# Kernel tuning notes

Measured on AMD Instinct MI355X. Metric: run time of the kernel, lower is better.

## Reference

```python
import jax, jax.numpy as jnp
import numpy as np

B_, C_, H_, W_ = 8, 128, 64, 64
OUT_ = 128
D_MODEL = C_ // 4        # 32, per-chunk channels fed to Mamba
D_STATE = 16
D_CONV = 4
D_INNER = 2 * D_MODEL    # expand=2 -> 64
DT_RANK = max(1, -(-D_MODEL // 16))  # ceil(32/16)=2
SE_RED = 2


def _ln(x, g, b):
    m = x.mean(-1, keepdims=True)
    v = jnp.var(x, axis=-1, keepdims=True)
    return (x - m) / jnp.sqrt(v + 1e-5) * g + b


def _mamba(u, in_W, conv_W, conv_b, xproj_W, dt_W, dt_b, A_log, D_p, out_W):
    # u: (B, L, d_model)
    Bsz, L, _ = u.shape
    xz = u @ in_W.T                                   # (B,L,2*d_inner)
    x, z = jnp.split(xz, 2, axis=-1)
    # causal depthwise conv1d along L
    xc = jnp.swapaxes(x, 1, 2)                        # (B,d_inner,L)
    xc = jax.lax.conv_general_dilated(
        xc, conv_W, (1,), [(D_CONV - 1, 0)],
        feature_group_count=D_INNER,
        dimension_numbers=('NCH', 'OIH', 'NCH'))
    x = jax.nn.silu(jnp.swapaxes(xc + conv_b[None, :, None], 1, 2))
    x_dbl = x @ xproj_W.T                             # (B,L,dt_rank+2*d_state)
    dt, Bm, Cm = jnp.split(x_dbl, [DT_RANK, DT_RANK + D_STATE], axis=-1)
    dt = jax.nn.softplus(dt @ dt_W.T + dt_b)          # (B,L,d_inner)
    A = -jnp.exp(A_log)                               # (d_inner,d_state)
    dA = jnp.exp(dt[..., None] * A)                   # (B,L,d_inner,d_state)
    dBu = dt[..., None] * Bm[:, :, None, :] * x[..., None]

    def step(h, inp):
        dA_t, dBu_t, C_t = inp
        h = dA_t * h + dBu_t                          # (B,d_inner,d_state)
        return h, jnp.einsum('bds,bs->bd', h, C_t)

    h0 = jnp.zeros((Bsz, D_INNER, D_STATE), dtype=x.dtype)
    _, ys = jax.lax.scan(step, h0, (jnp.swapaxes(dA, 0, 1), jnp.swapaxes(dBu, 0, 1), jnp.swapaxes(Cm, 0, 1)))
    y = jnp.swapaxes(ys, 0, 1) + x * D_p
    y = y * jax.nn.silu(z)
    return y @ out_W.T


def _branch(xi, skip_scale, se_W1, se_W2, mp):
    M1 = _mamba(xi, *mp)                              # (B,L,c)
    M2 = skip_scale * xi
    # SE: adaptive avg-pool over spatial == mean over tokens; cat over channels
    y = jnp.concatenate([M1, M2], axis=-1).mean(axis=1)   # (B,2c)
    y = jax.nn.sigmoid(jax.nn.relu(y @ se_W1.T) @ se_W2.T)
    g1, g2 = jnp.split(y, 2, axis=-1)
    return g1[:, None, :] * M1 + g2[:, None, :] * M2


def _pvm(x, norm_g, norm_b, proj_W, proj_b, skip_scale, se_W1, se_W2,
         in_W, conv_W, conv_b, xproj_W, dt_W, dt_b, A_log, D_p, out_W):
    B, C, H, W = x.shape
    L = H * W
    xf = jnp.swapaxes(x.reshape(B, C, L), 1, 2)       # (B,L,C)
    xn = _ln(xf, norm_g, norm_b)
    mp = (in_W, conv_W, conv_b, xproj_W, dt_W, dt_b, A_log, D_p, out_W)
    outs = [_branch(c, skip_scale, se_W1, se_W2, mp) for c in jnp.split(xn, 4, axis=2)]
    xm = jnp.concatenate(outs, axis=2)                # (B,L,C)
    xm = _ln(xm, norm_g, norm_b)
    xm = xm @ proj_W.T + proj_b                       # (B,L,out)
    return jnp.swapaxes(xm, 1, 2).reshape(B, proj_W.shape[0], H, W)


def setup_inputs():
    key = jax.random.key(0)
    ks = jax.random.split(key, 10)
    p = {}
    p['x'] = jax.random.normal(ks[0], (B_, C_, H_, W_), jnp.float32)
    p['norm_g'] = jnp.ones((C_,), jnp.float32)
    p['norm_b'] = jnp.zeros((C_,), jnp.float32)
    p['proj_W'] = jax.random.normal(ks[1], (OUT_, C_), jnp.float32) * 0.05
    p['proj_b'] = jnp.zeros((OUT_,), jnp.float32)
    p['skip_scale'] = jnp.ones((1,), jnp.float32)
    p['se_W1'] = jax.random.normal(ks[2], (SE_RED, 2 * D_MODEL), jnp.float32) * 0.1
    p['se_W2'] = jax.random.normal(ks[3], (2 * D_MODEL, SE_RED), jnp.float32) * 0.1
    p['in_W'] = jax.random.normal(ks[4], (2 * D_INNER, D_MODEL), jnp.float32) * 0.1
    p['conv_W'] = jax.random.normal(ks[5], (D_INNER, 1, D_CONV), jnp.float32) * 0.2
    p['conv_b'] = jnp.zeros((D_INNER,), jnp.float32)
    p['xproj_W'] = jax.random.normal(ks[6], (DT_RANK + 2 * D_STATE, D_INNER), jnp.float32) * 0.1
    p['dt_W'] = jax.random.normal(ks[7], (D_INNER, DT_RANK), jnp.float32) * 0.1
    p['dt_b'] = jnp.full((D_INNER,), -4.6, jnp.float32)  # softplus(-4.6) ~ 0.01 init dt
    p['A_log'] = jnp.log(jnp.broadcast_to(jnp.arange(1.0, D_STATE + 1.0, dtype=jnp.float32), (D_INNER, D_STATE)))
    p['D_p'] = jnp.ones((D_INNER,), jnp.float32)
    p['out_W'] = jax.random.normal(ks[8], (D_MODEL, D_INNER), jnp.float32) * 0.1
    return p


def reference(x, norm_g, norm_b, proj_W, proj_b, skip_scale, se_W1, se_W2,
              in_W, conv_W, conv_b, xproj_W, dt_W, dt_b, A_log, D_p, out_W):
    return _pvm(x, norm_g, norm_b, proj_W, proj_b, skip_scale, se_W1, se_W2,
                in_W, conv_W, conv_b, xproj_W, dt_W, dt_b, A_log, D_p, out_W)
```

## Files before the change

kernel.cpp:

```cpp
#include <hip/hip_runtime.h>
#include <math.h>

typedef _Float16 h16;

#define DEV static __device__ __forceinline__

constexpr int B_ = 8, C_ = 128, L_ = 4096, OUT_ = 128;
constexpr int NCH = 4, DM = 32, DS = 16, DI = 64;
constexpr int NI = 32;
constexpr int NSEG = 128;
constexpr int SL = L_ / NSEG;

DEV float sigmoidf_(float x) { return 1.f / (1.f + __expf(-x)); }
DEV float siluf_(float x) { return x * sigmoidf_(x); }
DEV float softplusf_(float x) { return (x > 20.f) ? x : __logf(1.f + __expf(x)); }

template <int CTRL>
DEV float dpp_add_(float x) {
  int v = __builtin_amdgcn_update_dpp(0, __float_as_int(x), CTRL, 0xf, 0xf, false);
  return x + __int_as_float(v);
}

typedef __attribute__((ext_vector_type(8))) _Float16 f16x8;
typedef __attribute__((ext_vector_type(4))) _Float16 f16x4;
typedef __attribute__((ext_vector_type(4))) float f32x4;

DEV void powladder_(float E, float* out) {
  float E2 = E * E;
  float E4 = E2 * E2;
  float E8 = E4 * E4;
  float E3 = E2 * E;
  out[0] = E;       out[1] = E2;      out[2] = E3;      out[3] = E4;
  out[4] = E4 * E;  out[5] = E4 * E2; out[6] = E4 * E3; out[7] = E8;
  out[8] = E8 * E;  out[9] = E8 * E2; out[10] = E8 * E3; out[11] = E8 * E4;
  out[12] = E8 * out[4]; out[13] = E8 * out[5]; out[14] = E8 * out[6];
  out[15] = E8 * E8;
}

DEV void powladder8_(float E, float* out) {
  float E2 = E * E, E3 = E2 * E, E4 = E2 * E2;
  out[0] = E; out[1] = E2; out[2] = E3; out[3] = E4;
  out[4] = E4 * E; out[5] = E4 * E2; out[6] = E4 * E3; out[7] = E4 * E4;
}

__global__ __launch_bounds__(256) void k0_wcvt(const float* __restrict__ in_W,
                                               const float* __restrict__ xproj_W,
                                               h16* __restrict__ WH) {
  int tid = blockIdx.x * 256 + threadIdx.x;
  if (tid < 4096) {
    WH[tid] = (h16)in_W[tid];
  } else if (tid < 4096 + 48 * 64) {
    int j = tid - 4096;
    int r = j >> 6;
    WH[tid] = (r < 34) ? (h16)xproj_W[r * 64 + (j & 63)] : (h16)0.f;
  }
}

__global__ __launch_bounds__(256) void k1_ln(const float* __restrict__ x,
                                             const float* __restrict__ gn,
                                             const float* __restrict__ bn,
                                             float* __restrict__ XN,
                                             h16* __restrict__ XNH,
                                             float* __restrict__ SUMXN) {
  int bid = blockIdx.x;
  int b = bid >> 6, tile = bid & 63;
  int t0 = tile * 64;
  int tid = threadIdx.x;
  __shared__ float xT[128][65];
  __shared__ float gnS[128], bnS[128];
  __shared__ float red[256];
  if (tid < 128) { gnS[tid] = gn[tid]; bnS[tid] = bn[tid]; }
  for (int k = tid; k < 8192; k += 256) {
    int c = k >> 6, tt = k & 63;
    xT[c][tt] = x[((size_t)(b * C_ + c)) * L_ + t0 + tt];
  }
  __syncthreads();
  {
    int tok = tid >> 2, q = tid & 3;
    float s = 0.f, qq = 0.f;
#pragma unroll
    for (int j = 0; j < 32; ++j) {
      float v = xT[q + 4 * j][tok];
      s += v; qq += v * v;
    }
    s = dpp_add_<0xB1>(s); qq = dpp_add_<0xB1>(qq);
    s = dpp_add_<0x4E>(s); qq = dpp_add_<0x4E>(qq);
    float m = s * (1.f / 128.f);
    float var = qq * (1.f / 128.f) - m * m;
    float rs = rsqrtf(var + 1e-5f);
#pragma unroll
    for (int j = 0; j < 32; ++j) {
      int c = q + 4 * j;
      float v = xT[c][tok];
      xT[c][tok] = (v - m) * rs * gnS[c] + bnS[c];
    }
  }
  __syncthreads();
  float acc = 0.f;
  int cfix = tid & 127;
  for (int k = tid; k < 8192; k += 256) {
    int tt = k >> 7, c = k & 127;
    float v = xT[c][tt];
    XN[((size_t)(b * L_ + t0 + tt)) * C_ + c] = v;
    acc += v;
  }
  for (int k = tid; k < 1024; k += 256) {
    int tt = k >> 4, c8 = (k & 15) * 8;
    f16x8 hv;
#pragma unroll
    for (int j = 0; j < 8; ++j) hv[j] = (_Float16)xT[c8 + j][tt];
    *(f16x8*)&XNH[((size_t)(b * L_ + t0 + tt)) * C_ + c8] = hv;
  }
  red[tid] = acc;
  __syncthreads();
  if (tid < 128) atomicAdd(&SUMXN[b * C_ + cfix], red[tid] + red[tid + 128]);
}

__global__ __launch_bounds__(256) void k2_prep(
    const h16* __restrict__ WH, const float* __restrict__ conv_W,
    const float* __restrict__ conv_b, const float* __restrict__ dt_W,
    const float* __restrict__ dt_b, const float* __restrict__ A_log,
    const h16* __restrict__ XNH, h16* __restrict__ SX2, h16* __restrict__ SDT2,
    h16* __restrict__ SB2, h16* __restrict__ SC2, h16* __restrict__ SZ2,
    float* __restrict__ Pp, float* __restrict__ Qp) {
  int bid = blockIdx.x;
  int i = bid >> 6, tile = bid & 63;
  int b = i >> 2, ch = i & 3;
  int t0 = tile * 64;
  int tid = threadIdx.x;
  int w = __builtin_amdgcn_readfirstlane(tid >> 6);
  int lane = tid & 63;

  __shared__ __attribute__((aligned(16))) union {
    struct {
      _Float16 uH[80][40];
      _Float16 w1H[64][40];
    } s;
    float xdS[64][36];
    _Float16 zL[64][88];
  } U;
  __shared__ __attribute__((aligned(16))) _Float16 preH[80][66];
  __shared__ __attribute__((aligned(16))) _Float16 xH[64][72];
  __shared__ __attribute__((aligned(16))) _Float16 w2H[48][72];
  __shared__ float convWS[64][4];
  __shared__ float dtWS[64][2];
  __shared__ float dtbS[64], cbS[64];

  convWS[tid >> 2][tid & 3] = conv_W[tid];
  if (tid < 128) dtWS[tid >> 1][tid & 1] = dt_W[tid];
  if (tid < 64) { dtbS[tid] = dt_b[tid]; cbS[tid] = conv_b[tid]; }
  const h16* xnh = XNH + (size_t)b * L_ * C_ + ch * DM;
  for (int k = tid; k < 320; k += 256) {
    int r = k >> 2, c8 = (k & 3) * 8;
    int tg = t0 - 3 + r;
    f16x8 v = {0, 0, 0, 0, 0, 0, 0, 0};
    if (r < 67 && tg >= 0) v = *(const f16x8*)&xnh[(size_t)tg * C_ + c8];
    *(f16x8*)&U.s.uH[r][c8] = v;
  }
  {
    int r = tid >> 2, c8 = (tid & 3) * 8;
    *(f16x8*)&U.s.w1H[r][c8] = *(const f16x8*)&WH[r * 32 + c8];
  }
  for (int k = tid; k < 384; k += 256) {
    int r = k >> 3, c8 = (k & 7) * 8;
    *(f16x8*)&w2H[r][c8] = *(const f16x8*)&WH[4096 + r * 64 + c8];
  }
  __syncthreads();

  int rsel = lane & 15, ksel = (lane >> 4) * 8;
  {
    int nt = w;
    f16x8 bf = *(const f16x8*)&U.s.w1H[nt * 16 + rsel][ksel];
    int row0q = (lane >> 4) << 2;
    int col = nt * 16 + rsel;
#pragma unroll
    for (int mt = 0; mt < 5; ++mt) {
      f16x8 af = *(const f16x8*)&U.s.uH[mt * 16 + rsel][ksel];
      f32x4 acc = {0.f, 0.f, 0.f, 0.f};
      acc = __builtin_amdgcn_mfma_f32_16x16x32_f16(af, bf, acc, 0, 0, 0);
      int row0 = mt * 16 + row0q;
#pragma unroll
      for (int r = 0; r < 4; ++r) preH[row0 + r][col] = (_Float16)acc[r];
    }
  }
  f32x4 zacc[4];
  {
    f16x8 bf = *(const f16x8*)&U.s.uH[3 + w * 16 + rsel][ksel];
#pragma unroll
    for (int mt = 0; mt < 4; ++mt) {
      f16x8 af = *(const f16x8*)&WH[(size_t)(64 + mt * 16 + rsel) * 32 + ksel];
      f32x4 acc = {0.f, 0.f, 0.f, 0.f};
      zacc[mt] = __builtin_amdgcn_mfma_f32_16x16x32_f16(af, bf, acc, 0, 0, 0);
    }
  }
  __syncthreads();

  h16* SXp = SX2 + ((size_t)i * L_ + t0) * DI;
  for (int k = tid; k < 4096; k += 256) {
    int r = k >> 6, d = k & 63;
    float v = cbS[d];
#pragma unroll
    for (int j = 0; j < 4; ++j) v = fmaf(convWS[d][j], (float)preH[r + j][d], v);
    v = siluf_(v);
    xH[r][d] = (_Float16)v;
    SXp[(size_t)r * DI + d] = (h16)v;
  }
  __syncthreads();

  {
    int mt = w;
    f16x8 a0 = *(const f16x8*)&xH[mt * 16 + rsel][ksel];
    f16x8 a1 = *(const f16x8*)&xH[mt * 16 + rsel][32 + ksel];
    int row0 = mt * 16 + ((lane >> 4) << 2);
#pragma unroll
    for (int nt = 0; nt < 3; ++nt) {
      f16x8 b0 = *(const f16x8*)&w2H[nt * 16 + rsel][ksel];
      f16x8 b1 = *(const f16x8*)&w2H[nt * 16 + rsel][32 + ksel];
      f32x4 acc = {0.f, 0.f, 0.f, 0.f};
      acc = __builtin_amdgcn_mfma_f32_16x16x32_f16(a0, b0, acc, 0, 0, 0);
      acc = __builtin_amdgcn_mfma_f32_16x16x32_f16(a1, b1, acc, 0, 0, 0);
      int col = nt * 16 + rsel;
      if (col < 34) {
#pragma unroll
        for (int r = 0; r < 4; ++r) U.xdS[row0 + r][col] = acc[r];
      }
    }
  }
  __syncthreads();

  h16* dtL = (h16*)&preH[0][0];
  h16* SDTp = SDT2 + ((size_t)i * L_ + t0) * DI;
  for (int k = tid; k < 4096; k += 256) {
    int d = k & 63, r = k >> 6;
    float raw = fmaf(U.xdS[r][0], dtWS[d][0], fmaf(U.xdS[r][1], dtWS[d][1], dtbS[d]));
    float dtv = softplusf_(raw);
    dtL[r * 66 + d] = (_Float16)dtv;
    SDTp[(size_t)r * DI + d] = (h16)dtv;
  }
  h16* SBp = SB2 + ((size_t)i * L_ + t0) * DS;
  h16* SCp = SC2 + ((size_t)i * L_ + t0) * DS;
  for (int k = tid; k < 1024; k += 256) {
    int s = k & 15, r = k >> 4;
    SBp[(size_t)r * DS + s] = (h16)U.xdS[r][2 + s];
    SCp[(size_t)r * DS + s] = (h16)U.xdS[r][18 + s];
  }
  __syncthreads();

  {
    int seg = w >> 1, shalf = w & 1;
    int s0 = shalf * 8;
    float Av[16];
#pragma unroll
    for (int s = 0; s < 16; ++s) Av[s] = -__expf(A_log[lane * 16 + s]);
    float A0 = Av[0];
    bool okf = true;
#pragma unroll
    for (int s = 0; s < 16; ++s)
      okf &= fabsf(Av[s] - (float)(s + 1) * A0) <= 1e-4f * fabsf(Av[s]);
    int fastp = __all(okf ? 1 : 0);
    float h[8];
#pragma unroll
    for (int j = 0; j < 8; ++j) h[j] = 0.f;
    float sdt = 0.f;
    int rowbase = seg * SL;
    for (int t = 0; t < SL; ++t) {
      int row = rowbase + t;
      float dt = (float)dtL[row * 66 + lane];
      float xv = (float)xH[row][lane];
      float dtx = dt * xv;
      float dA[8];
      if (fastp) {
        powladder8_(__expf(A0 * dt), dA);
        if (shalf) {
          float E8 = dA[7];
#pragma unroll
          for (int j = 0; j < 8; ++j) dA[j] *= E8;
        }
      } else {
#pragma unroll
        for (int j = 0; j < 8; ++j) dA[j] = __expf(Av[s0 + j] * dt);
      }
      const float* brow = &U.xdS[row][2 + s0];
#pragma unroll
      for (int j = 0; j < 8; ++j) h[j] = fmaf(dA[j], h[j], dtx * brow[j]);
      sdt += dt;
    }
    float P[8];
    if (fastp) {
      powladder8_(__expf(A0 * sdt), P);
      if (shalf) {
        float E8 = P[7];
#pragma unroll
        for (int j = 0; j < 8; ++j) P[j] *= E8;
      }
    } else {
#pragma unroll
      for (int j = 0; j < 8; ++j) P[j] = __expf(Av[s0 + j] * sdt);
    }
    int segg = tile * 2 + seg;
    size_t base = (((size_t)i * DI + lane) * NSEG + segg) * DS + s0;
    *(float4*)(Pp + base) = *(float4*)&P[0];
    *(float4*)(Pp + base + 4) = *(float4*)&P[4];
    *(float4*)(Qp + base) = *(float4*)&h[0];
    *(float4*)(Qp + base + 4) = *(float4*)&h[4];
  }
  __syncthreads();

  {
    int tok = w * 16 + rsel;
    int zq = (lane >> 4) << 2;
#pragma unroll
    for (int mt = 0; mt < 4; ++mt) {
      f16x4 pk;
#pragma unroll
      for (int r = 0; r < 4; ++r) pk[r] = (_Float16)siluf_(zacc[mt][r]);
      *(f16x4*)&U.zL[tok][mt * 16 + zq] = pk;
    }
  }
  __syncthreads();
  h16* SZp = SZ2 + ((size_t)i * L_ + t0) * DI;
  for (int k = tid; k < 512; k += 256) {
    int r = k >> 3, dblk = (k & 7) * 8;
    f16x8 v = *(const f16x8*)&U.zL[r][dblk];
    *(f16x8*)&SZp[(size_t)r * DI + dblk] = v;
  }
}

__global__ __launch_bounds__(256) void k3b_comb(float* __restrict__ Pp,
                                                const float* __restrict__ Qp) {
  int g = blockIdx.x * 256 + threadIdx.x;
  int s = g & 15;
  int r = g >> 4;
  size_t base = (size_t)r * NSEG * DS + s;
  float H = 0.f;
  for (int sb = 0; sb < NSEG; sb += 8) {
    float Pv[8], Qv[8];
#pragma unroll
    for (int j = 0; j < 8; ++j) {
      size_t a = base + (size_t)(sb + j) * DS;
      Pv[j] = Pp[a];
      Qv[j] = Qp[a];
    }
#pragma unroll
    for (int j = 0; j < 8; ++j) {
      size_t a = base + (size_t)(sb + j) * DS;
      Pp[a] = H;
      H = fmaf(Pv[j], H, Qv[j]);
    }
  }
}

__global__ __launch_bounds__(256) void k3c_scan(
    const float* __restrict__ A_log, const h16* __restrict__ SDT2,
    const h16* __restrict__ SX2, const h16* __restrict__ SB2,
    const h16* __restrict__ SC2, const h16* __restrict__ SZ2,
    const float* __restrict__ D_p, const float* __restrict__ H0p,
    h16* __restrict__ YS2, float* __restrict__ SUMYF) {
  int bid = blockIdx.x;
  int i = bid >> 5, sg = bid & 31;
  int tid = threadIdx.x;
  int w = tid >> 6, lane = tid & 63;
  int seg = sg * 4 + w;
  int t0 = seg * SL;
  __shared__ float rowS[4][SL][36];
  {
    int tk = lane & 31, hf = lane >> 5;
    const h16* p = (hf ? SC2 : SB2) + ((size_t)i * L_ + t0 + tk) * DS;
    float4 r0 = *(const float4*)p;
    float4 r1 = *(const float4*)(p + 8);
    const h16* hp0 = (const h16*)&r0;
    const h16* hp1 = (const h16*)&r1;
#pragma unroll
    for (int s = 0; s < 8; ++s) {
      rowS[w][tk][hf * 16 + s] = (float)hp0[s];
      rowS[w][tk][hf * 16 + 8 + s] = (float)hp1[s];
    }
  }
  __syncthreads();
  float Av[16];
#pragma unroll
  for (int s = 0; s < 16; ++s) Av[s] = -__expf(A_log[lane * 16 + s]);
  float A0 = Av[0];
  bool okf = true;
#pragma unroll
  for (int s = 0; s < 16; ++s) okf &= fabsf(Av[s] - (float)(s + 1) * A0) <= 1e-4f * fabsf(Av[s]);
  int fastp = __all(okf ? 1 : 0);
  float Dp = D_p[lane];
  float h[16];
  {
    size_t base = (((size_t)i * DI + lane) * NSEG + seg) * DS;
#pragma unroll
    for (int j = 0; j < 4; ++j) *(float4*)&h[4 * j] = *(const float4*)(H0p + base + 4 * j);
  }
  const h16* pdt = SDT2 + ((size_t)i * L_ + t0) * DI + lane;
  const h16* pxx = SX2 + ((size_t)i * L_ + t0) * DI + lane;
  const h16* pzz = SZ2 + ((size_t)i * L_ + t0) * DI + lane;
  h16* pys = YS2 + ((size_t)i * L_ + t0) * DI + lane;
  float dtc = (float)pdt[0], xvc = (float)pxx[0], zvc = (float)pzz[0];
  float sum = 0.f;
  for (int t = 0; t < SL; ++t) {
    float dt = dtc, xv = xvc, zv = zvc;
    if (t < SL - 1) {
      dtc = (float)pdt[(t + 1) * DI];
      xvc = (float)pxx[(t + 1) * DI];
      zvc = (float)pzz[(t + 1) * DI];
    }
    const float* row = &rowS[w][t][0];
    float Bv[16], Cv[16];
#pragma unroll
    for (int j = 0; j < 4; ++j) {
      *(float4*)&Bv[4 * j] = *(const float4*)(row + 4 * j);
      *(float4*)&Cv[4 * j] = *(const float4*)(row + 16 + 4 * j);
    }
    float dtx = dt * xv;
    float dA[16];
    if (fastp) {
      powladder_(__expf(A0 * dt), dA);
    } else {
#pragma unroll
      for (int s = 0; s < 16; ++s) dA[s] = __expf(Av[s] * dt);
    }
    float y0 = 0.f, y1 = 0.f, y2 = 0.f, y3 = 0.f;
#pragma unroll
    for (int s = 0; s < 16; s += 4) {
      h[s] = fmaf(dA[s], h[s], dtx * Bv[s]);       y0 = fmaf(h[s], Cv[s], y0);
      h[s + 1] = fmaf(dA[s + 1], h[s + 1], dtx * Bv[s + 1]); y1 = fmaf(h[s + 1], Cv[s + 1], y1);
      h[s + 2] = fmaf(dA[s + 2], h[s + 2], dtx * Bv[s + 2]); y2 = fmaf(h[s + 2], Cv[s + 2], y2);
      h[s + 3] = fmaf(dA[s + 3], h[s + 3], dtx * Bv[s + 3]); y3 = fmaf(h[s + 3], Cv[s + 3], y3);
    }
    float y = (y0 + y1) + (y2 + y3);
    float yf = fmaf(xv, Dp, y) * zv;
    pys[(size_t)t * DI] = (h16)yf;
    sum += yf;
  }
  atomicAdd(&SUMYF[i * DI + lane], sum);
}

__global__ __launch_bounds__(64) void k4_gates(
    const float* __restrict__ out_W, const float* __restrict__ se_W1,
    const float* __restrict__ se_W2, const float* __restrict__ skip_p,
    const float* __restrict__ SUMYF, const float* __restrict__ SUMXN,
    float* __restrict__ GATES) {
  int i = blockIdx.x;
  int b = i >> 2, ch = i & 3;
  int tid = threadIdx.x;
  __shared__ float syS[64], catS[64], seS[2];
  syS[tid] = SUMYF[i * DI + tid];
  __syncthreads();
  float invL = 1.f / (float)L_;
  if (tid < 32) {
    float acc = 0.f;
#pragma unroll
    for (int dd = 0; dd < 64; ++dd) acc = fmaf(syS[dd], out_W[tid * 64 + dd], acc);
    catS[tid] = acc * invL;
  } else {
    int c = tid - 32;
    catS[tid] = skip_p[0] * SUMXN[b * C_ + ch * DM + c] * invL;
  }
  __syncthreads();
  if (tid < 2) {
    float acc = 0.f;
#pragma unroll
    for (int k = 0; k < 64; ++k) acc = fmaf(catS[k], se_W1[tid * 64 + k], acc);
    seS[tid] = fmaxf(acc, 0.f);
  }
  __syncthreads();
  float gg = fmaf(seS[0], se_W2[tid * 2 + 0], seS[1] * se_W2[tid * 2 + 1]);
  GATES[i * DI + tid] = sigmoidf_(gg);
}

__global__ __launch_bounds__(256) void k56_comb_proj(
    const float* __restrict__ out_W, const float* __restrict__ skip_p,
    const float* __restrict__ GATES, const h16* __restrict__ YS2,
    const float* __restrict__ gn, const float* __restrict__ bn,
    const float* __restrict__ proj_W, const float* __restrict__ proj_b,
    const float* __restrict__ XN, float* __restrict__ out) {
  int bid = blockIdx.x;
  int b = bid >> 6, tile = bid & 63;
  int t0 = tile * 64;
  int tid = threadIdx.x;
  int w = __builtin_amdgcn_readfirstlane(tid >> 6);
  int lane = tid & 63;
  __shared__ __attribute__((aligned(16))) union {
    float xmS[64][132];
    _Float16 projH[128][136];
  } U;
  __shared__ __attribute__((aligned(16))) union {
    struct {
      _Float16 yH[64][72];
      _Float16 owH[32][72];
    } pre;
    _Float16 xmH[64][136];
  } V;
  __shared__ float gAll[4][64];
  __shared__ float gnS[128], bnS[128];

  if (tid < 128) { gnS[tid] = gn[tid]; bnS[tid] = bn[tid]; }
  const float* xm = XN + (size_t)b * L_ * C_;
  for (int k = tid; k < 8192; k += 256) {
    int tt = k >> 7, c = k & 127;
    U.xmS[tt][c] = xm[(size_t)(t0 + tt) * C_ + c];
  }
  if (tid < 256) gAll[tid >> 6][tid & 63] = GATES[(b * 4 + (tid >> 6)) * DI + (tid & 63)];
  for (int k = tid; k < 2048; k += 256) V.pre.owH[k >> 6][k & 63] = (_Float16)out_W[k];

  int rsel = lane & 15, ksel = (lane >> 4) * 8;
  float skip = skip_p[0];
  for (int ch = 0; ch < 4; ++ch) {
    const h16* py = YS2 + ((size_t)(b * 4 + ch) * L_ + t0) * DI;
    for (int k = tid; k < 512; k += 256) {
      int tt = k >> 3, dblk = (k & 7) * 8;
      *(f16x8*)&V.pre.yH[tt][dblk] = *(const f16x8*)&py[(size_t)tt * DI + dblk];
    }
    __syncthreads();
    f16x8 a0 = *(const f16x8*)&V.pre.yH[w * 16 + rsel][ksel];
    f16x8 a1 = *(const f16x8*)&V.pre.yH[w * 16 + rsel][32 + ksel];
    int row0 = w * 16 + ((lane >> 4) << 2);
#pragma unroll
    for (int nt = 0; nt < 2; ++nt) {
      f16x8 b0 = *(const f16x8*)&V.pre.owH[nt * 16 + rsel][ksel];
      f16x8 b1 = *(const f16x8*)&V.pre.owH[nt * 16 + rsel][32 + ksel];
      f32x4 acc = {0.f, 0.f, 0.f, 0.f};
      acc = __builtin_amdgcn_mfma_f32_16x16x32_f16(a0, b0, acc, 0, 0, 0);
      acc = __builtin_amdgcn_mfma_f32_16x16x32_f16(a1, b1, acc, 0, 0, 0);
      int o = nt * 16 + rsel;
      float g1 = gAll[ch][o], g2s = gAll[ch][32 + o] * skip;
      int cc = ch * 32 + o;
#pragma unroll
      for (int r = 0; r < 4; ++r) {
        int tok = row0 + r;
        U.xmS[tok][cc] = g1 * acc[r] + g2s * U.xmS[tok][cc];
      }
    }
    __syncthreads();
  }

  {
    int tok = tid >> 2, q = tid & 3;
    float s = 0.f, qq = 0.f;
#pragma unroll
    for (int j = 0; j < 32; ++j) {
      float v = U.xmS[tok][4 * j + q];
      s += v; qq += v * v;
    }
    s = dpp_add_<0xB1>(s); qq = dpp_add_<0xB1>(qq);
    s = dpp_add_<0x4E>(s); qq = dpp_add_<0x4E>(qq);
    float m = s * (1.f / 128.f);
    float var = qq * (1.f / 128.f) - m * m;
    float rs = rsqrtf(var + 1e-5f);
#pragma unroll
    for (int j = 0; j < 32; ++j) {
      int c = 4 * j + q;
      float v = U.xmS[tok][c];
      U.xmS[tok][c] = (v - m) * rs * gnS[c] + bnS[c];
    }
  }
  __syncthreads();
  for (int k = tid; k < 1024; k += 256) {
    int tt = k >> 4, cblk = (k & 15) * 8;
    float4 v0 = *(const float4*)&U.xmS[tt][cblk];
    float4 v1 = *(const float4*)&U.xmS[tt][cblk + 4];
    f16x8 hv;
    hv[0] = (_Float16)v0.x; hv[1] = (_Float16)v0.y;
    hv[2] = (_Float16)v0.z; hv[3] = (_Float16)v0.w;
    hv[4] = (_Float16)v1.x; hv[5] = (_Float16)v1.y;
    hv[6] = (_Float16)v1.z; hv[7] = (_Float16)v1.w;
    *(f16x8*)&V.xmH[tt][cblk] = hv;
  }
  __syncthreads();
  for (int k = tid; k < 2048; k += 256) {
    int o = k >> 4, cblk = (k & 15) * 8;
    const float* wp = proj_W + o * 128 + cblk;
    float4 v0 = *(const float4*)wp;
    float4 v1 = *(const float4*)(wp + 4);
    f16x8 hv;
    hv[0] = (_Float16)v0.x; hv[1] = (_Float16)v0.y;
    hv[2] = (_Float16)v0.z; hv[3] = (_Float16)v0.w;
    hv[4] = (_Float16)v1.x; hv[5] = (_Float16)v1.y;
    hv[6] = (_Float16)v1.z; hv[7] = (_Float16)v1.w;
    *(f16x8*)&U.projH[o][cblk] = hv;
  }
  __syncthreads();
  f16x8 af[4];
#pragma unroll
  for (int kc = 0; kc < 4; ++kc)
    af[kc] = *(const f16x8*)&V.xmH[w * 16 + rsel][kc * 32 + ksel];
  int row0 = w * 16 + ((lane >> 4) << 2);
#pragma unroll
  for (int nt = 0; nt < 8; ++nt) {
    int o = nt * 16 + rsel;
    float pb = proj_b[o];
    f32x4 acc = {pb, pb, pb, pb};
#pragma unroll
    for (int kc = 0; kc < 4; ++kc) {
      f16x8 bf = *(const f16x8*)&U.projH[o][kc * 32 + ksel];
      acc = __builtin_amdgcn_mfma_f32_16x16x32_f16(af[kc], bf, acc, 0, 0, 0);
    }
    *(float4*)&out[((size_t)(b * OUT_ + o)) * L_ + t0 + row0] =
        make_float4(acc[0], acc[1], acc[2], acc[3]);
  }
}

extern "C" void kernel_launch(void* const* d_in, const int* in_sizes, int n_in,
                              void* d_out, int out_size, void* d_ws, size_t ws_size,
                              hipStream_t stream) {
  const float* x = (const float*)d_in[0];
  const float* norm_g = (const float*)d_in[1];
  const float* norm_b = (const float*)d_in[2];
  const float* proj_W = (const float*)d_in[3];
  const float* proj_b = (const float*)d_in[4];
  const float* skip = (const float*)d_in[5];
  const float* se_W1 = (const float*)d_in[6];
  const float* se_W2 = (const float*)d_in[7];
  const float* in_W = (const float*)d_in[8];
  const float* conv_W = (const float*)d_in[9];
  const float* conv_b = (const float*)d_in[10];
  const float* xproj_W = (const float*)d_in[11];
  const float* dt_W = (const float*)d_in[12];
  const float* dt_b = (const float*)d_in[13];
  const float* A_log = (const float*)d_in[14];
  const float* D_p = (const float*)d_in[15];
  const float* out_W = (const float*)d_in[16];
  float* out = (float*)d_out;

  float* XN = (float*)d_ws;
  float* SUMYF = XN + (size_t)B_ * L_ * C_;
  float* SUMXN = SUMYF + NI * DI;
  float* GATES = SUMXN + B_ * C_;
  float* Pp = GATES + NI * DI;
  float* Qp = Pp + (size_t)NI * DI * NSEG * DS;
  h16* YS2 = (h16*)(Qp + (size_t)NI * DI * NSEG * DS);
  h16* SX2 = YS2 + (size_t)NI * L_ * DI;
  h16* SDT2 = SX2 + (size_t)NI * L_ * DI;
  h16* SB2 = SDT2 + (size_t)NI * L_ * DI;
  h16* SC2 = SB2 + (size_t)NI * L_ * DS;
  h16* SZ2 = SC2 + (size_t)NI * L_ * DS;
  h16* XNH = SZ2 + (size_t)NI * L_ * DI;
  h16* WH = XNH + (size_t)B_ * L_ * C_;

  hipMemsetAsync(SUMYF, 0, (size_t)(NI * DI + B_ * C_) * sizeof(float), stream);
  k0_wcvt<<<28, 256, 0, stream>>>(in_W, xproj_W, WH);
  k1_ln<<<B_ * 64, 256, 0, stream>>>(x, norm_g, norm_b, XN, XNH, SUMXN);
  k2_prep<<<NI * 64, 256, 0, stream>>>(WH, conv_W, conv_b, dt_W, dt_b, A_log,
                                       XNH, SX2, SDT2, SB2, SC2, SZ2, Pp, Qp);
  k3b_comb<<<128, 256, 0, stream>>>(Pp, Qp);
  k3c_scan<<<NI * 32, 256, 0, stream>>>(A_log, SDT2, SX2, SB2, SC2, SZ2, D_p,
                                        Pp, YS2, SUMYF);
  k4_gates<<<NI, 64, 0, stream>>>(out_W, se_W1, se_W2, skip, SUMYF, SUMXN, GATES);
  k56_comb_proj<<<B_ * 64, 256, 0, stream>>>(out_W, skip, GATES, YS2, norm_g,
                                             norm_b, proj_W, proj_b, XN, out);
}
```

Before: 214.1 us.

## Drop fp32 normalized buffer, fold gate computation into projection kernel, remove memset

```diff
diff --git a/kernel.cpp b/kernel.cpp
--- a/kernel.cpp
+++ b/kernel.cpp
@@ -45,11 +45,13 @@
 
 __global__ __launch_bounds__(256) void k0_wcvt(const float* __restrict__ in_W,
                                                const float* __restrict__ xproj_W,
-                                               h16* __restrict__ WH) {
+                                               h16* __restrict__ WH,
+                                               float* __restrict__ Zp) {
   int tid = blockIdx.x * 256 + threadIdx.x;
+  if (tid < 3072) Zp[tid] = 0.f;
   if (tid < 4096) {
     WH[tid] = (h16)in_W[tid];
-  } else if (tid < 4096 + 48 * 64) {
+  } else {
     int j = tid - 4096;
     int r = j >> 6;
     WH[tid] = (r < 34) ? (h16)xproj_W[r * 64 + (j & 63)] : (h16)0.f;
@@ -59,7 +61,6 @@
 __global__ __launch_bounds__(256) void k1_ln(const float* __restrict__ x,
                                              const float* __restrict__ gn,
                                              const float* __restrict__ bn,
-                                             float* __restrict__ XN,
                                              h16* __restrict__ XNH,
                                              float* __restrict__ SUMXN) {
   int bid = blockIdx.x;
@@ -100,9 +101,7 @@
   int cfix = tid & 127;
   for (int k = tid; k < 8192; k += 256) {
     int tt = k >> 7, c = k & 127;
-    float v = xT[c][tt];
-    XN[((size_t)(b * L_ + t0 + tt)) * C_ + c] = v;
-    acc += v;
+    acc += xT[c][tt];
   }
   for (int k = tid; k < 1024; k += 256) {
     int tt = k >> 4, c8 = (k & 15) * 8;
@@ -139,7 +138,7 @@
     float xdS[64][36];
     _Float16 zL[64][88];
   } U;
-  __shared__ __attribute__((aligned(16))) _Float16 preH[80][66];
+  __shared__ __attribute__((aligned(16))) _Float16 preH[80][68];
   __shared__ __attribute__((aligned(16))) _Float16 xH[64][72];
   __shared__ __attribute__((aligned(16))) _Float16 w2H[48][72];
   __shared__ float convWS[64][4];
@@ -234,7 +233,7 @@
     int d = k & 63, r = k >> 6;
     float raw = fmaf(U.xdS[r][0], dtWS[d][0], fmaf(U.xdS[r][1], dtWS[d][1], dtbS[d]));
     float dtv = softplusf_(raw);
-    dtL[r * 66 + d] = (_Float16)dtv;
+    dtL[r * 68 + d] = (_Float16)dtv;
     SDTp[(size_t)r * DI + d] = (h16)dtv;
   }
   h16* SBp = SB2 + ((size_t)i * L_ + t0) * DS;
@@ -265,7 +264,7 @@
     int rowbase = seg * SL;
     for (int t = 0; t < SL; ++t) {
       int row = rowbase + t;
-      float dt = (float)dtL[row * 66 + lane];
+      float dt = (float)dtL[row * 68 + lane];
       float xv = (float)xH[row][lane];
       float dtx = dt * xv;
       float dA[8];
@@ -436,45 +435,14 @@
   atomicAdd(&SUMYF[i * DI + lane], sum);
 }
 
-__global__ __launch_bounds__(64) void k4_gates(
-    const float* __restrict__ out_W, const float* __restrict__ se_W1,
-    const float* __restrict__ se_W2, const float* __restrict__ skip_p,
-    const float* __restrict__ SUMYF, const float* __restrict__ SUMXN,
-    float* __restrict__ GATES) {
-  int i = blockIdx.x;
-  int b = i >> 2, ch = i & 3;
-  int tid = threadIdx.x;
-  __shared__ float syS[64], catS[64], seS[2];
-  syS[tid] = SUMYF[i * DI + tid];
-  __syncthreads();
-  float invL = 1.f / (float)L_;
-  if (tid < 32) {
-    float acc = 0.f;
-#pragma unroll
-    for (int dd = 0; dd < 64; ++dd) acc = fmaf(syS[dd], out_W[tid * 64 + dd], acc);
-    catS[tid] = acc * invL;
-  } else {
-    int c = tid - 32;
-    catS[tid] = skip_p[0] * SUMXN[b * C_ + ch * DM + c] * invL;
-  }
-  __syncthreads();
-  if (tid < 2) {
-    float acc = 0.f;
-#pragma unroll
-    for (int k = 0; k < 64; ++k) acc = fmaf(catS[k], se_W1[tid * 64 + k], acc);
-    seS[tid] = fmaxf(acc, 0.f);
-  }
-  __syncthreads();
-  float gg = fmaf(seS[0], se_W2[tid * 2 + 0], seS[1] * se_W2[tid * 2 + 1]);
-  GATES[i * DI + tid] = sigmoidf_(gg);
-}
-
 __global__ __launch_bounds__(256) void k56_comb_proj(
     const float* __restrict__ out_W, const float* __restrict__ skip_p,
-    const float* __restrict__ GATES, const h16* __restrict__ YS2,
-    const float* __restrict__ gn, const float* __restrict__ bn,
-    const float* __restrict__ proj_W, const float* __restrict__ proj_b,
-    const float* __restrict__ XN, float* __restrict__ out) {
+    const float* __restrict__ se_W1, const float* __restrict__ se_W2,
+    const float* __restrict__ SUMYF, const float* __restrict__ SUMXN,
+    const h16* __restrict__ YS2, const float* __restrict__ gn,
+    const float* __restrict__ bn, const float* __restrict__ proj_W,
+    const float* __restrict__ proj_b, const h16* __restrict__ XNH,
+    float* __restrict__ out) {
   int bid = blockIdx.x;
   int b = bid >> 6, tile = bid & 63;
   int t0 = tile * 64;
@@ -494,15 +462,46 @@
   } V;
   __shared__ float gAll[4][64];
   __shared__ float gnS[128], bnS[128];
+  float* catS = (float*)&V.pre.yH[0][0];
+  float* seL = catS + 256;
 
   if (tid < 128) { gnS[tid] = gn[tid]; bnS[tid] = bn[tid]; }
-  const float* xm = XN + (size_t)b * L_ * C_;
-  for (int k = tid; k < 8192; k += 256) {
-    int tt = k >> 7, c = k & 127;
-    U.xmS[tt][c] = xm[(size_t)(t0 + tt) * C_ + c];
-  }
-  if (tid < 256) gAll[tid >> 6][tid & 63] = GATES[(b * 4 + (tid >> 6)) * DI + (tid & 63)];
   for (int k = tid; k < 2048; k += 256) V.pre.owH[k >> 6][k & 63] = (_Float16)out_W[k];
+  const h16* xmh = XNH + (size_t)b * L_ * C_;
+  for (int k = tid; k < 1024; k += 256) {
+    int tt = k >> 4, c8 = (k & 15) * 8;
+    f16x8 hv = *(const f16x8*)&xmh[(size_t)(t0 + tt) * C_ + c8];
+#pragma unroll
+    for (int j = 0; j < 8; ++j) U.xmS[tt][c8 + j] = (float)hv[j];
+  }
+  {
+    int ch = tid >> 6, j = tid & 63;
+    float invL = 1.f / (float)L_;
+    if (j < 32) {
+      const float* sy = SUMYF + (b * 4 + ch) * DI;
+      const float* ow = out_W + j * 64;
+      float acc = 0.f;
+#pragma unroll
+      for (int dd = 0; dd < 64; ++dd) acc = fmaf(sy[dd], ow[dd], acc);
+      catS[ch * 64 + j] = acc * invL;
+    } else {
+      catS[ch * 64 + j] = skip_p[0] * SUMXN[b * C_ + ch * DM + (j - 32)] * invL;
+    }
+  }
+  __syncthreads();
+  if (tid < 8) {
+    int ch = tid >> 1, r = tid & 1;
+    float acc = 0.f;
+#pragma unroll
+    for (int k = 0; k < 64; ++k) acc = fmaf(catS[ch * 64 + k], se_W1[r * 64 + k], acc);
+    seL[tid] = fmaxf(acc, 0.f);
+  }
+  __syncthreads();
+  {
+    int ch = tid >> 6, j = tid & 63;
+    gAll[ch][j] = sigmoidf_(fmaf(seL[ch * 2], se_W2[j * 2], seL[ch * 2 + 1] * se_W2[j * 2 + 1]));
+  }
+  __syncthreads();
 
   int rsel = lane & 15, ksel = (lane >> 4) * 8;
   float skip = skip_p[0];
@@ -623,11 +622,9 @@
   const float* out_W = (const float*)d_in[16];
   float* out = (float*)d_out;
 
-  float* XN = (float*)d_ws;
-  float* SUMYF = XN + (size_t)B_ * L_ * C_;
+  float* SUMYF = (float*)d_ws;
   float* SUMXN = SUMYF + NI * DI;
-  float* GATES = SUMXN + B_ * C_;
-  float* Pp = GATES + NI * DI;
+  float* Pp = SUMXN + B_ * C_;
   float* Qp = Pp + (size_t)NI * DI * NSEG * DS;
   h16* YS2 = (h16*)(Qp + (size_t)NI * DI * NSEG * DS);
   h16* SX2 = YS2 + (size_t)NI * L_ * DI;
@@ -638,15 +635,14 @@
   h16* XNH = SZ2 + (size_t)NI * L_ * DI;
   h16* WH = XNH + (size_t)B_ * L_ * C_;
 
-  hipMemsetAsync(SUMYF, 0, (size_t)(NI * DI + B_ * C_) * sizeof(float), stream);
-  k0_wcvt<<<28, 256, 0, stream>>>(in_W, xproj_W, WH);
-  k1_ln<<<B_ * 64, 256, 0, stream>>>(x, norm_g, norm_b, XN, XNH, SUMXN);
+  k0_wcvt<<<28, 256, 0, stream>>>(in_W, xproj_W, WH, SUMYF);
+  k1_ln<<<B_ * 64, 256, 0, stream>>>(x, norm_g, norm_b, XNH, SUMXN);
   k2_prep<<<NI * 64, 256, 0, stream>>>(WH, conv_W, conv_b, dt_W, dt_b, A_log,
                                        XNH, SX2, SDT2, SB2, SC2, SZ2, Pp, Qp);
   k3b_comb<<<128, 256, 0, stream>>>(Pp, Qp);
   k3c_scan<<<NI * 32, 256, 0, stream>>>(A_log, SDT2, SX2, SB2, SC2, SZ2, D_p,
                                         Pp, YS2, SUMYF);
-  k4_gates<<<NI, 64, 0, stream>>>(out_W, se_W1, se_W2, skip, SUMYF, SUMXN, GATES);
-  k56_comb_proj<<<B_ * 64, 256, 0, stream>>>(out_W, skip, GATES, YS2, norm_g,
-                                             norm_b, proj_W, proj_b, XN, out);
-}
+  k56_comb_proj<<<B_ * 64, 256, 0, stream>>>(out_W, skip, se_W1, se_W2, SUMYF,
+                                             SUMXN, YS2, norm_g, norm_b, proj_W,
+                                             proj_b, XNH, out);
+}
```

New measurement: 214.0 us. No clear change (-0.0%).
